# Kernel optimization log

Measured on AMD Instinct MI355X. Metric: run time of the kernel, lower is better.

The kernel has to match this reference:

```python
import jax, jax.numpy as jnp
import numpy as np

H = 8          # attention heads
DV = 32        # per-head dim for view2global (256/8)
DS = 32        # per-head dim for scenepoint2global (256/8)
DG = 512       # n_feat_global_out
DIN = 256      # n_feat_view_in == n_feat_scenepoint_in
EPS = 1e-5


def layernorm(x, scale, bias):
    m = jnp.mean(x, axis=-1, keepdims=True)
    v = jnp.var(x, axis=-1, keepdims=True)
    return (x - m) / jnp.sqrt(v + EPS) * scale + bias


def gatv2_star(x_src, x_tgt, Wl, bl, Wr, br, att, out_bias, heads, dim):
    """GATv2Conv over a star graph: every source node -> single target node.
    x_src: [N, Din], x_tgt: [1, Din]. Returns [1, heads*dim]."""
    xl = (x_src @ Wl + bl).reshape(-1, heads, dim)          # [N,H,D] messages
    xr = (x_tgt @ Wr + br).reshape(1, heads, dim)           # [1,H,D]
    e = jax.nn.leaky_relu(xl + xr, negative_slope=0.2)      # [N,H,D]
    logits = jnp.einsum('nhd,hd->nh', e, att)               # [N,H]
    alpha = jax.nn.softmax(logits, axis=0)                  # softmax over edges per head
    out = jnp.einsum('nh,nhd->hd', alpha, xl).reshape(1, heads * dim)
    return out + out_bias


def setup_inputs() -> dict:
    key = jax.random.key(0)
    ks = jax.random.split(key, 24)
    s = 0.05
    inp = {
        'view_features': jax.random.normal(ks[0], (4096, DIN), jnp.float32),
        'scenepoint_features': jax.random.normal(ks[1], (262144, DIN), jnp.float32),
        'prev_global_features': jax.random.normal(ks[2], (1, DG), jnp.float32),
        # norm_and_proj_global2view: LayerNorm(512) -> ReLU -> Linear(512,256)
        'g2v_ln_s': jnp.ones((DG,), jnp.float32),
        'g2v_ln_b': jnp.zeros((DG,), jnp.float32),
        'g2v_W': jax.random.normal(ks[3], (DG, DIN), jnp.float32) * s,
        'g2v_b': jnp.zeros((DIN,), jnp.float32),
        # norm_and_proj_global2scenepoint
        'g2s_ln_s': jnp.ones((DG,), jnp.float32),
        'g2s_ln_b': jnp.zeros((DG,), jnp.float32),
        'g2s_W': jax.random.normal(ks[4], (DG, DIN), jnp.float32) * s,
        'g2s_b': jnp.zeros((DIN,), jnp.float32),
        # GATv2Conv view2global
        'v_Wl': jax.random.normal(ks[5], (DIN, H * DV), jnp.float32) * s,
        'v_bl': jnp.zeros((H * DV,), jnp.float32),
        'v_Wr': jax.random.normal(ks[6], (DIN, H * DV), jnp.float32) * s,
        'v_br': jnp.zeros((H * DV,), jnp.float32),
        'v_att': jax.random.normal(ks[7], (H, DV), jnp.float32) * s,
        'v_bias': jnp.zeros((H * DV,), jnp.float32),
        # GATv2Conv scenepoint2global
        's_Wl': jax.random.normal(ks[8], (DIN, H * DS), jnp.float32) * s,
        's_bl': jnp.zeros((H * DS,), jnp.float32),
        's_Wr': jax.random.normal(ks[9], (DIN, H * DS), jnp.float32) * s,
        's_br': jnp.zeros((H * DS,), jnp.float32),
        's_att': jax.random.normal(ks[10], (H, DS), jnp.float32) * s,
        's_bias': jnp.zeros((H * DS,), jnp.float32),
        # norm_pre_mlp + mlp (single Linear 512->512, no norm inside mlp)
        'pre_ln_s': jnp.ones((DG,), jnp.float32),
        'pre_ln_b': jnp.zeros((DG,), jnp.float32),
        'mlp_W': jax.random.normal(ks[11], (DG, DG), jnp.float32) * s,
        'mlp_b': jnp.zeros((DG,), jnp.float32),
    }
    return inp


def reference(view_features, scenepoint_features, prev_global_features,
              g2v_ln_s, g2v_ln_b, g2v_W, g2v_b,
              g2s_ln_s, g2s_ln_b, g2s_W, g2s_b,
              v_Wl, v_bl, v_Wr, v_br, v_att, v_bias,
              s_Wl, s_bl, s_Wr, s_br, s_att, s_bias,
              pre_ln_s, pre_ln_b, mlp_W, mlp_b):
    # target-node input features for each star graph
    xt_v = jax.nn.relu(layernorm(prev_global_features, g2v_ln_s, g2v_ln_b)) @ g2v_W + g2v_b
    xt_s = jax.nn.relu(layernorm(prev_global_features, g2s_ln_s, g2s_ln_b)) @ g2s_W + g2s_b
    v2g = gatv2_star(view_features, xt_v, v_Wl, v_bl, v_Wr, v_br, v_att, v_bias, H, DV)
    s2g = gatv2_star(scenepoint_features, xt_s, s_Wl, s_bl, s_Wr, s_br, s_att, s_bias, H, DS)
    x = jnp.concatenate([v2g, s2g], axis=1)                 # [1, 512] == n_feat_global_out
    x = prev_global_features + x                            # stateful residual
    x_skip = x
    x = jax.nn.relu(layernorm(x, pre_ln_s, pre_ln_b))       # norm_pre_mlp + relu
    x = x @ mlp_W + mlp_b                                   # mlp (0 hidden layers)
    return x_skip + x
```

## Files before the change

kernel.cpp:

```cpp
#include <hip/hip_runtime.h>
#include <hip/hip_bf16.h>

typedef unsigned short ushort_t;
typedef __attribute__((ext_vector_type(8))) short bf16x8;
typedef __attribute__((ext_vector_type(4))) float f32x4;

#define NSCENE 4096
#define NVIEW  64
#define NBUCK  16
#define TPB    8

#define WS_XR    0
#define WS_ACC   512
#define WS_PACK  10240
#define WS_NEED_PACKED ((size_t)WS_PACK*4 + 2u*65536u*2u)

__device__ __forceinline__ float bf2f(ushort_t u) {
    union { unsigned int i; float f; } v; v.i = ((unsigned int)u) << 16; return v.f;
}
__device__ __forceinline__ ushort_t f2bf(float f) {
    union { float f; unsigned int i; } v; v.f = f;
    unsigned int x = v.i;
    return (ushort_t)((x + 0x7fffu + ((x >> 16) & 1u)) >> 16);
}
template<bool F32>
__device__ __forceinline__ float ldT(const void* p, int i) {
    if (F32) return ((const float*)p)[i];
    return bf2f(((const ushort_t*)p)[i]);
}
__device__ __forceinline__ bool is_bf16(const void* det) {
    return ((const ushort_t*)det)[0] == 0x3F80u;
}
__device__ __forceinline__ void async16(const void* g, void* lds) {
    __builtin_amdgcn_global_load_lds(
        (const __attribute__((address_space(1))) unsigned int*)g,
        (__attribute__((address_space(3))) unsigned int*)lds, 16, 0, 0);
}
__device__ __forceinline__ float qsum16(float x) {
    union { float f; int i; } a, b;
#define QS_STEP(CTRL) { a.f = x; b.i = __builtin_amdgcn_update_dpp(0, a.i, CTRL, 0xF, 0xF, true); x += b.f; }
    QS_STEP(0x128)
    QS_STEP(0x124)
    QS_STEP(0x122)
    QS_STEP(0x121)
#undef QS_STEP
    return x;
}

template<bool F32>
__global__ __launch_bounds__(512)
void prep_pack_k(const void* __restrict__ prev,
                 const void* __restrict__ lns_v, const void* __restrict__ lnb_v,
                 const void* __restrict__ W_v,   const void* __restrict__ b_v,
                 const void* __restrict__ Wr_v,  const void* __restrict__ br_v,
                 const void* __restrict__ lns_s, const void* __restrict__ lnb_s,
                 const void* __restrict__ W_s,   const void* __restrict__ b_s,
                 const void* __restrict__ Wr_s,  const void* __restrict__ br_s,
                 const void* __restrict__ v_Wl,  const void* __restrict__ s_Wl,
                 float* __restrict__ xr, float* __restrict__ accSO,
                 ushort_t* __restrict__ pack)
{
    if (is_bf16(lns_v) == F32) return;
    const int bid = blockIdx.x;
    const int t = threadIdx.x;

    if (bid >= 2) {
        const int pb = bid - 2;
        const int br = pb >> 4;
        const void* Wl = br ? s_Wl : v_Wl;
        const int o0 = (pb & 15)*4096 + t*8;
        const int lane = (o0 >> 3) & 63, kk = (o0 >> 9) & 7, ntw = o0 >> 12;
        const int quad = lane >> 4, li = lane & 15;
        const int col  = (ntw >> 1)*32 + (ntw & 1)*16 + li;
        union { ushort_t u[8]; int4 v; } t_;
#pragma unroll
        for (int j = 0; j < 8; j++) {
            const int r = kk*32 + quad*8 + j;
            t_.u[j] = F32 ? f2bf(((const float*)Wl)[r*256 + col])
                          : ((const ushort_t*)Wl)[r*256 + col];
        }
        *(int4*)(pack + br*65536 + o0) = t_.v;
        return;
    }

    const int br = bid;
    const void* lns = br ? lns_s : lns_v;
    const void* lnb = br ? lnb_s : lnb_v;
    const void* W   = br ? W_s   : W_v;
    const void* bb  = br ? b_s   : b_v;
    const void* Wr  = br ? Wr_s  : Wr_v;
    const void* brr = br ? br_s  : br_v;
#pragma unroll
    for (int b = 0; b < NBUCK; b++)
        for (int i = t; i < 264; i += 512) accSO[b*528 + br*264 + i] = 0.f;

    __shared__ float g[512];
    __shared__ float xt[256];
    __shared__ float red[16];
    __shared__ float stats[2];
    __shared__ float part[512];

    float a0 = ldT<F32>(prev, t);
    float s1 = a0, s2 = a0*a0;
#pragma unroll
    for (int s = 1; s < 64; s <<= 1) { s1 += __shfl_xor(s1, s); s2 += __shfl_xor(s2, s); }
    if ((t & 63) == 0) { red[t >> 6] = s1; red[8 + (t >> 6)] = s2; }
    __syncthreads();
    if (t == 0) {
        float a = 0.f, q = 0.f;
        for (int i = 0; i < 8; i++) { a += red[i]; q += red[8 + i]; }
        float mean = a / 512.f;
        stats[0] = mean;
        stats[1] = rsqrtf(q / 512.f - mean*mean + 1e-5f);
    }
    __syncthreads();
    g[t] = fmaxf((a0 - stats[0])*stats[1]*ldT<F32>(lns, t) + ldT<F32>(lnb, t), 0.f);
    __syncthreads();

    const int c = t & 255, kh = t >> 8;
    {
        const int base = kh * 256;
        float acc = 0.f;
        for (int ii = 0; ii < 256; ii += 32) {
            float wv[32];
#pragma unroll
            for (int u = 0; u < 32; u++) wv[u] = ldT<F32>(W, (base + ii + u)*256 + c);
#pragma unroll
            for (int u = 0; u < 32; u++) acc += g[base + ii + u] * wv[u];
        }
        part[t] = acc;
    }
    __syncthreads();
    if (t < 256) xt[t] = part[t] + part[t + 256] + ldT<F32>(bb, t);
    __syncthreads();
    {
        const int b2 = kh * 128;
        float acc2 = 0.f;
        for (int ii = 0; ii < 128; ii += 32) {
            float wv[32];
#pragma unroll
            for (int u = 0; u < 32; u++) wv[u] = ldT<F32>(Wr, (b2 + ii + u)*256 + c);
#pragma unroll
            for (int u = 0; u < 32; u++) acc2 += xt[b2 + ii + u] * wv[u];
        }
        part[t] = acc2;
    }
    __syncthreads();
    if (t < 256) xr[br*256 + t] = part[t] + part[t + 256] + ldT<F32>(brr, t);
}

template<bool F32, bool PACKED>
__global__ __launch_bounds__(512, 4)
void gat_k(const void* __restrict__ view_x, const void* __restrict__ scene_x,
           const ushort_t* __restrict__ pack,
           const void* __restrict__ v_Wl, const void* __restrict__ s_Wl,
           const float* __restrict__ xr_all,
           const void* __restrict__ v_bl, const void* __restrict__ s_bl,
           const void* __restrict__ v_att, const void* __restrict__ s_att,
           const void* __restrict__ det,
           float* __restrict__ accSO)
{
    if (is_bf16(det) == F32) return;

    const int tid  = threadIdx.x;
    const int wave = tid >> 6;
    const int lane = tid & 63;
    const int quad = lane >> 4;
    const int li   = lane & 15;
    const int bid  = blockIdx.x;

    __shared__ __align__(16) ushort_t alds[2][64 * 256];

    for (int seg = 0; seg < 2; ++seg) {
        if (seg == 1 && bid >= NVIEW) break;
        const bool scene = (seg == 0);
        const void* xsrc     = scene ? scene_x : view_x;
        const ushort_t* pkw  = pack + (scene ? 65536 : 0) + wave*2*4096;
        const void* Wl       = scene ? s_Wl : v_Wl;
        const float* xrp     = xr_all + (scene ? 256 : 0);
        const void* blp      = scene ? s_bl  : v_bl;
        const void* attp     = scene ? s_att : v_att;
        float* accR          = accSO + (bid & (NBUCK - 1))*528 + (scene ? 264 : 0);
        const int t0         = scene ? bid*TPB : bid;
        const int nT         = scene ? TPB : 1;

        auto loadB = [&](int nt, int k) -> bf16x8 {
            if constexpr (PACKED) {
                return *(const bf16x8*)(pkw + nt*4096 + k*512 + lane*8);
            } else {
                union { ushort_t u[8]; bf16x8 v; } tmp;
#pragma unroll
                for (int j = 0; j < 8; j++) {
                    const int idx = (k*32 + quad*8 + j)*256 + (wave*32 + nt*16 + li);
                    tmp.u[j] = F32 ? f2bf(((const float*)Wl)[idx]) : ((const ushort_t*)Wl)[idx];
                }
                return tmp.v;
            }
        };

        auto stage = [&](ushort_t* dst, int tile) {
            const int l5 = lane >> 5, g2 = lane & 31;
#pragma unroll
            for (int j = 0; j < 4; j++) {
                const int ci  = wave*4 + j;
                const int row = 2*ci + l5;
                const int g   = (g2 & 24) | ((g2 & 7) ^ (row & 7));
                const size_t gelem = (size_t)(tile*64 + row)*256 + g*8;
                if (F32) {
                    const float* p = (const float*)xsrc + gelem;
                    float4 a = *(const float4*)p, b = *(const float4*)(p + 4);
                    union { ushort_t u[8]; int4 v; } t_;
                    t_.u[0]=f2bf(a.x); t_.u[1]=f2bf(a.y); t_.u[2]=f2bf(a.z); t_.u[3]=f2bf(a.w);
                    t_.u[4]=f2bf(b.x); t_.u[5]=f2bf(b.y); t_.u[6]=f2bf(b.z); t_.u[7]=f2bf(b.w);
                    *(int4*)(&dst[ci*512 + lane*8]) = t_.v;
                } else {
                    async16((const ushort_t*)xsrc + gelem, &dst[ci*512]);
                }
            }
        };

        const int c0 = wave*32 + li;
        const float xr0 = xrp[c0],            xr1 = xrp[c0 + 16];
        const float at0 = ldT<F32>(attp, c0), at1 = ldT<F32>(attp, c0 + 16);
        const float bl0 = ldT<F32>(blp, c0),  bl1 = ldT<F32>(blp, c0 + 16);

        stage(alds[0], t0);
        __syncthreads();
        int cur = 0;

        float Ssum = 0.f, oa0 = 0.f, oa1 = 0.f;

        for (int ti = 0; ti < nT; ++ti) {
            const bool pf = (ti + 1 < nT);

            f32x4 acc[4][2] = {};
            const ushort_t* aldc = alds[cur];
#pragma unroll 2
            for (int k = 0; k < 8; k++) {
                const int gq = k*4 + quad;
                const int gp = (gq & 24) | ((gq & 7) ^ (li & 7));
                bf16x8 a0 = *(const bf16x8*)(&aldc[(  0 + li)*256 + gp*8]);
                bf16x8 a1 = *(const bf16x8*)(&aldc[( 16 + li)*256 + gp*8]);
                bf16x8 a2 = *(const bf16x8*)(&aldc[( 32 + li)*256 + gp*8]);
                bf16x8 a3 = *(const bf16x8*)(&aldc[( 48 + li)*256 + gp*8]);
                const bf16x8 B0 = loadB(0, k);
                const bf16x8 B1 = loadB(1, k);
                __builtin_amdgcn_s_setprio(1);
                acc[0][0] = __builtin_amdgcn_mfma_f32_16x16x32_bf16(a0, B0, acc[0][0], 0, 0, 0);
                acc[1][0] = __builtin_amdgcn_mfma_f32_16x16x32_bf16(a1, B0, acc[1][0], 0, 0, 0);
                acc[2][0] = __builtin_amdgcn_mfma_f32_16x16x32_bf16(a2, B0, acc[2][0], 0, 0, 0);
                acc[3][0] = __builtin_amdgcn_mfma_f32_16x16x32_bf16(a3, B0, acc[3][0], 0, 0, 0);
                acc[0][1] = __builtin_amdgcn_mfma_f32_16x16x32_bf16(a0, B1, acc[0][1], 0, 0, 0);
                acc[1][1] = __builtin_amdgcn_mfma_f32_16x16x32_bf16(a1, B1, acc[1][1], 0, 0, 0);
                acc[2][1] = __builtin_amdgcn_mfma_f32_16x16x32_bf16(a2, B1, acc[2][1], 0, 0, 0);
                acc[3][1] = __builtin_amdgcn_mfma_f32_16x16x32_bf16(a3, B1, acc[3][1], 0, 0, 0);
                __builtin_amdgcn_s_setprio(0);
            }

            if (!F32 && pf) stage(alds[cur ^ 1], t0 + ti + 1);
            float4 sa[4], sb[4];
            if (F32 && pf) {
                const int l5 = lane >> 5, g2 = lane & 31;
#pragma unroll
                for (int j = 0; j < 4; j++) {
                    const int row = 2*(wave*4 + j) + l5;
                    const int g   = (g2 & 24) | ((g2 & 7) ^ (row & 7));
                    const float* p = (const float*)xsrc
                                   + (size_t)((t0 + ti + 1)*64 + row)*256 + g*8;
                    sa[j] = *(const float4*)p;
                    sb[j] = *(const float4*)(p + 4);
                }
            }

#pragma unroll
            for (int m = 0; m < 4; m++) {
#pragma unroll
                for (int r = 0; r < 4; r++) {
                    float x0 = acc[m][0][r] + bl0;
                    float x1 = acc[m][1][r] + bl1;
                    float e0 = x0 + xr0; e0 = e0 > 0.f ? e0 : 0.2f*e0;
                    float e1 = x1 + xr1; e1 = e1 > 0.f ? e1 : 0.2f*e1;
                    float p = qsum16(at0*e0 + at1*e1);
                    float w = __expf(fminf(p, 60.f));
                    Ssum += w;
                    oa0 += w * x0;
                    oa1 += w * x1;
                }
            }

            if (F32 && pf) {
#pragma unroll
                for (int j = 0; j < 4; j++) {
                    const int ci = wave*4 + j;
                    union { ushort_t u[8]; int4 v; } t_;
                    t_.u[0]=f2bf(sa[j].x); t_.u[1]=f2bf(sa[j].y);
                    t_.u[2]=f2bf(sa[j].z); t_.u[3]=f2bf(sa[j].w);
                    t_.u[4]=f2bf(sb[j].x); t_.u[5]=f2bf(sb[j].y);
                    t_.u[6]=f2bf(sb[j].z); t_.u[7]=f2bf(sb[j].w);
                    *(int4*)(&alds[cur ^ 1][ci*512 + lane*8]) = t_.v;
                }
            }

            __syncthreads();
            cur ^= 1;
        }

        float S = Ssum, o0 = oa0, o1 = oa1;
        S  += __shfl_xor(S, 16);  S  += __shfl_xor(S, 32);
        o0 += __shfl_xor(o0, 16); o0 += __shfl_xor(o0, 32);
        o1 += __shfl_xor(o1, 16); o1 += __shfl_xor(o1, 32);
        if (lane == 0) atomicAdd(&accR[wave], S);
        if (lane < 16) {
            atomicAdd(&accR[8 + wave*32 + lane],      o0);
            atomicAdd(&accR[8 + wave*32 + 16 + lane], o1);
        }
    }
}

template<bool F32>
__global__ __launch_bounds__(512)
void tail_k(const float* __restrict__ accSO,
            const void* __restrict__ prev,
            const void* __restrict__ v_bias, const void* __restrict__ s_bias,
            const void* __restrict__ pre_s, const void* __restrict__ pre_b,
            const void* __restrict__ W, const void* __restrict__ mb,
            const void* __restrict__ det,
            void* __restrict__ out)
{
    if (is_bf16(det) == F32) return;
    const int t = threadIdx.x;
    const int branch = t >> 8, c = t & 255, h = c >> 5;

    __shared__ float xsk[512];
    __shared__ float xn[512];
    __shared__ float part[512];
    __shared__ float red[16];
    __shared__ float stats[2];

    float S = 0.f, o = 0.f;
#pragma unroll
    for (int b = 0; b < NBUCK; b++) {
        S += accSO[b*528 + branch*264 + h];
        o += accSO[b*528 + branch*264 + 8 + c];
    }
    const void* bias = branch ? s_bias : v_bias;
    float xv = ldT<F32>(prev, t) + o / S + ldT<F32>(bias, c);
    xsk[t] = xv;

    float s1 = xv, s2 = xv*xv;
#pragma unroll
    for (int s = 1; s < 64; s <<= 1) { s1 += __shfl_xor(s1, s); s2 += __shfl_xor(s2, s); }
    if ((t & 63) == 0) { red[t >> 6] = s1; red[8 + (t >> 6)] = s2; }
    __syncthreads();
    if (t == 0) {
        float a = 0.f, q = 0.f;
        for (int i = 0; i < 8; i++) { a += red[i]; q += red[8 + i]; }
        float mean = a / 512.f;
        stats[0] = mean;
        stats[1] = rsqrtf(q / 512.f - mean*mean + 1e-5f);
    }
    __syncthreads();
    xn[t] = fmaxf((xv - stats[0])*stats[1]*ldT<F32>(pre_s, t) + ldT<F32>(pre_b, t), 0.f);
    __syncthreads();

    const int cc = blockIdx.x*64 + (t & 63);
    const int b0 = (t >> 6) * 64;
    float acc = 0.f;
    for (int ii = 0; ii < 64; ii += 32) {
        float wv[32];
#pragma unroll
        for (int u = 0; u < 32; u++) wv[u] = ldT<F32>(W, (b0 + ii + u)*512 + cc);
#pragma unroll
        for (int u = 0; u < 32; u++) acc += xn[b0 + ii + u] * wv[u];
    }
    part[t] = acc;
    __syncthreads();
    if (t < 64) {
        const int cf = blockIdx.x*64 + t;
        float r = xsk[cf] + ldT<F32>(mb, cf);
#pragma unroll
        for (int j = 0; j < 8; j++) r += part[j*64 + t];
        if (F32) ((float*)out)[cf] = r;
        else     ((ushort_t*)out)[cf] = f2bf(r);
    }
}

extern "C" void kernel_launch(void* const* d_in, const int* in_sizes, int n_in,
                              void* d_out, int out_size, void* d_ws, size_t ws_size,
                              hipStream_t stream)
{
    const void* view_x  = d_in[0];
    const void* scene_x = d_in[1];
    const void* prev    = d_in[2];
    const void* g2v_lns = d_in[3];
    const void* g2v_lnb = d_in[4];
    const void* g2v_W   = d_in[5];
    const void* g2v_b   = d_in[6];
    const void* g2s_lns = d_in[7];
    const void* g2s_lnb = d_in[8];
    const void* g2s_W   = d_in[9];
    const void* g2s_b   = d_in[10];
    const void* v_Wl    = d_in[11];
    const void* v_bl    = d_in[12];
    const void* v_Wr    = d_in[13];
    const void* v_br    = d_in[14];
    const void* v_att   = d_in[15];
    const void* v_bias  = d_in[16];
    const void* s_Wl    = d_in[17];
    const void* s_bl    = d_in[18];
    const void* s_Wr    = d_in[19];
    const void* s_br    = d_in[20];
    const void* s_att   = d_in[21];
    const void* s_bias  = d_in[22];
    const void* pre_s   = d_in[23];
    const void* pre_b   = d_in[24];
    const void* mlp_W   = d_in[25];
    const void* mlp_b   = d_in[26];

    float* wsf      = (float*)d_ws;
    float* xr       = wsf + WS_XR;
    float* accSO    = wsf + WS_ACC;
    ushort_t* packW = (ushort_t*)(wsf + WS_PACK);

    const bool packed = (ws_size >= WS_NEED_PACKED);
    const int prep_blocks = packed ? 34 : 2;

    prep_pack_k<false><<<dim3(prep_blocks), dim3(512), 0, stream>>>(prev,
                                              g2v_lns, g2v_lnb, g2v_W, g2v_b, v_Wr, v_br,
                                              g2s_lns, g2s_lnb, g2s_W, g2s_b, s_Wr, s_br,
                                              v_Wl, s_Wl, xr, accSO, packW);
    prep_pack_k<true><<<dim3(prep_blocks), dim3(512), 0, stream>>>(prev,
                                              g2v_lns, g2v_lnb, g2v_W, g2v_b, v_Wr, v_br,
                                              g2s_lns, g2s_lnb, g2s_W, g2s_b, s_Wr, s_br,
                                              v_Wl, s_Wl, xr, accSO, packW);
    if (packed) {
        gat_k<false, true><<<dim3(512), dim3(512), 0, stream>>>(view_x, scene_x, packW,
                                                  v_Wl, s_Wl, xr, v_bl, s_bl, v_att, s_att,
                                                  g2v_lns, accSO);
        gat_k<true, true><<<dim3(512), dim3(512), 0, stream>>>(view_x, scene_x, packW,
                                                  v_Wl, s_Wl, xr, v_bl, s_bl, v_att, s_att,
                                                  g2v_lns, accSO);
    } else {
        gat_k<false, false><<<dim3(512), dim3(512), 0, stream>>>(view_x, scene_x, packW,
                                                  v_Wl, s_Wl, xr, v_bl, s_bl, v_att, s_att,
                                                  g2v_lns, accSO);
        gat_k<true, false><<<dim3(512), dim3(512), 0, stream>>>(view_x, scene_x, packW,
                                                  v_Wl, s_Wl, xr, v_bl, s_bl, v_att, s_att,
                                                  g2v_lns, accSO);
    }
    tail_k<false><<<dim3(8), dim3(512), 0, stream>>>(accSO, prev, v_bias, s_bias,
                                                     pre_s, pre_b, mlp_W, mlp_b,
                                                     g2v_lns, d_out);
    tail_k<true><<<dim3(8), dim3(512), 0, stream>>>(accSO, prev, v_bias, s_bias,
                                                    pre_s, pre_b, mlp_W, mlp_b,
                                                    g2v_lns, d_out);
}
```

Measured before the change: 464.0 us.

## Launch only dtype-matching kernels and interleave scene tile assignment across blocks

The host now reads the input byte size to decide whether inputs are f32 or bf16, and launches only the matching prep, GAT and tail kernels instead of both variants. Before, both variants ran every call, which doubled the work. Scene tiles are also handed out with a stride of the grid size (bid + ti*NBLK) rather than as a contiguous run per block. This spreads concurrent memory accesses across the whole array. If in_sizes is missing, both variants still run as before.

```diff
diff --git a/kernel.cpp b/kernel.cpp
--- a/kernel.cpp
+++ b/kernel.cpp
@@ -8,6 +8,7 @@
 #define NSCENE 4096
 #define NVIEW  64
 #define NBUCK  16
+#define NBLK   512
 #define TPB    8
 
 #define WS_XR    0
@@ -181,8 +182,8 @@
         const void* blp      = scene ? s_bl  : v_bl;
         const void* attp     = scene ? s_att : v_att;
         float* accR          = accSO + (bid & (NBUCK - 1))*528 + (scene ? 264 : 0);
-        const int t0         = scene ? bid*TPB : bid;
         const int nT         = scene ? TPB : 1;
+        auto tileOf = [&](int ti) { return scene ? (bid + ti*NBLK) : bid; };
 
         auto loadB = [&](int nt, int k) -> bf16x8 {
             if constexpr (PACKED) {
@@ -224,7 +225,7 @@
         const float at0 = ldT<F32>(attp, c0), at1 = ldT<F32>(attp, c0 + 16);
         const float bl0 = ldT<F32>(blp, c0),  bl1 = ldT<F32>(blp, c0 + 16);
 
-        stage(alds[0], t0);
+        stage(alds[0], tileOf(0));
         __syncthreads();
         int cur = 0;
 
@@ -257,16 +258,17 @@
                 __builtin_amdgcn_s_setprio(0);
             }
 
-            if (!F32 && pf) stage(alds[cur ^ 1], t0 + ti + 1);
+            if (!F32 && pf) stage(alds[cur ^ 1], tileOf(ti + 1));
             float4 sa[4], sb[4];
             if (F32 && pf) {
                 const int l5 = lane >> 5, g2 = lane & 31;
+                const int tnx = tileOf(ti + 1);
 #pragma unroll
                 for (int j = 0; j < 4; j++) {
                     const int row = 2*(wave*4 + j) + l5;
                     const int g   = (g2 & 24) | ((g2 & 7) ^ (row & 7));
                     const float* p = (const float*)xsrc
-                                   + (size_t)((t0 + ti + 1)*64 + row)*256 + g*8;
+                                   + (size_t)(tnx*64 + row)*256 + g*8;
                     sa[j] = *(const float4*)p;
                     sb[j] = *(const float4*)(p + 4);
                 }
@@ -425,33 +427,46 @@
     const bool packed = (ws_size >= WS_NEED_PACKED);
     const int prep_blocks = packed ? 34 : 2;
 
-    prep_pack_k<false><<<dim3(prep_blocks), dim3(512), 0, stream>>>(prev,
+    const bool sz_f32  = (in_sizes && in_sizes[0] == 4096*256*4);
+    const bool sz_bf16 = (in_sizes && in_sizes[0] == 4096*256*2);
+    const bool run_f32  = !sz_bf16;
+    const bool run_bf16 = !sz_f32;
+
+    if (run_bf16)
+        prep_pack_k<false><<<dim3(prep_blocks), dim3(512), 0, stream>>>(prev,
                                               g2v_lns, g2v_lnb, g2v_W, g2v_b, v_Wr, v_br,
                                               g2s_lns, g2s_lnb, g2s_W, g2s_b, s_Wr, s_br,
                                               v_Wl, s_Wl, xr, accSO, packW);
-    prep_pack_k<true><<<dim3(prep_blocks), dim3(512), 0, stream>>>(prev,
+    if (run_f32)
+        prep_pack_k<true><<<dim3(prep_blocks), dim3(512), 0, stream>>>(prev,
                                               g2v_lns, g2v_lnb, g2v_W, g2v_b, v_Wr, v_br,
                                               g2s_lns, g2s_lnb, g2s_W, g2s_b, s_Wr, s_br,
                                               v_Wl, s_Wl, xr, accSO, packW);
     if (packed) {
-        gat_k<false, true><<<dim3(512), dim3(512), 0, stream>>>(view_x, scene_x, packW,
+        if (run_bf16)
+            gat_k<false, true><<<dim3(NBLK), dim3(512), 0, stream>>>(view_x, scene_x, packW,
                                                   v_Wl, s_Wl, xr, v_bl, s_bl, v_att, s_att,
                                                   g2v_lns, accSO);
-        gat_k<true, true><<<dim3(512), dim3(512), 0, stream>>>(view_x, scene_x, packW,
+        if (run_f32)
+            gat_k<true, true><<<dim3(NBLK), dim3(512), 0, stream>>>(view_x, scene_x, packW,
                                                   v_Wl, s_Wl, xr, v_bl, s_bl, v_att, s_att,
                                                   g2v_lns, accSO);
     } else {
-        gat_k<false, false><<<dim3(512), dim3(512), 0, stream>>>(view_x, scene_x, packW,
+        if (run_bf16)
+            gat_k<false, false><<<dim3(NBLK), dim3(512), 0, stream>>>(view_x, scene_x, packW,
                                                   v_Wl, s_Wl, xr, v_bl, s_bl, v_att, s_att,
                                                   g2v_lns, accSO);
-        gat_k<true, false><<<dim3(512), dim3(512), 0, stream>>>(view_x, scene_x, packW,
+        if (run_f32)
+            gat_k<true, false><<<dim3(NBLK), dim3(512), 0, stream>>>(view_x, scene_x, packW,
                                                   v_Wl, s_Wl, xr, v_bl, s_bl, v_att, s_att,
                                                   g2v_lns, accSO);
     }
-    tail_k<false><<<dim3(8), dim3(512), 0, stream>>>(accSO, prev, v_bias, s_bias,
+    if (run_bf16)
+        tail_k<false><<<dim3(8), dim3(512), 0, stream>>>(accSO, prev, v_bias, s_bias,
                                                      pre_s, pre_b, mlp_W, mlp_b,
                                                      g2v_lns, d_out);
-    tail_k<true><<<dim3(8), dim3(512), 0, stream>>>(accSO, prev, v_bias, s_bias,
+    if (run_f32)
+        tail_k<true><<<dim3(8), dim3(512), 0, stream>>>(accSO, prev, v_bias, s_bias,
                                                     pre_s, pre_b, mlp_W, mlp_b,
                                                     g2v_lns, d_out);
 }
```

New measurement: 462.0 us. No clear change (-0.4%).
